# Optimization experiments

Hardware: AMD Instinct MI355X
Metric: run time of the kernel (lower is better)

The kernel has to match this reference:

```python
import jax, jax.numpy as jnp
import numpy as np

HIDDEN = 384
NDIM = 3
N_POINTS = 100000
N_SUPER = 2048
MAX_DEG = 32
RADIUS = 0.045
INPUT_DIM = 3


def _sincos_embed(coords):
    # ContinuousSincosEmbed: dim=384, ndim=3 -> 128 channels per spatial dim (64 sin + 64 cos)
    eff = HIDDEN // NDIM  # 128
    omega = jnp.arange(0, eff, 2, dtype=jnp.float32) / eff
    freq = 1.0 / (10000.0 ** omega)  # [eff//2]
    out = coords[..., None] * freq  # [..., ndim, eff//2]
    emb = jnp.concatenate([jnp.sin(out), jnp.cos(out)], axis=-1)  # [..., ndim, eff]
    return emb.reshape(coords.shape[:-1] + (HIDDEN,))


def _radius_neighbors(pos, sn_idx):
    # numpy preprocessing equivalent of torch_geometric.nn.pool.radius with
    # max_num_neighbors=MAX_DEG; fixed-size padded [S, K] output + validity mask.
    nbr = np.zeros((N_SUPER, MAX_DEG), np.int32)
    mask = np.zeros((N_SUPER, MAX_DEG), bool)
    pos2 = (pos ** 2).sum(-1)
    r2 = RADIUS * RADIUS
    chunk = 128
    for i0 in range(0, N_SUPER, chunk):
        sp = pos[sn_idx[i0:i0 + chunk]]
        d2 = (sp ** 2).sum(-1)[:, None] + pos2[None, :] - 2.0 * (sp @ pos.T)
        within = d2 <= r2
        for j in range(sp.shape[0]):
            idx = np.nonzero(within[j])[0][:MAX_DEG]
            nbr[i0 + j, :len(idx)] = idx
            mask[i0 + j, :len(idx)] = True
    return nbr, mask


def setup_inputs() -> dict:
    rng = np.random.default_rng(0)
    pos = rng.random((N_POINTS, NDIM)).astype(np.float32)
    sn_idx = np.sort(rng.choice(N_POINTS, N_SUPER, replace=False)).astype(np.int32)
    nbr, mask = _radius_neighbors(pos, sn_idx)
    key = jax.random.key(0)
    ks = jax.random.split(key, 6)
    s = 0.02  # truncnormal002 init scale
    return {
        "input_pos": jnp.asarray(pos),
        "input_feat": jax.random.normal(ks[0], (N_POINTS, INPUT_DIM), jnp.float32),
        "supernode_idx": jnp.asarray(sn_idx),
        "neighbor_idx": jnp.asarray(nbr),
        "neighbor_mask": jnp.asarray(mask),
        "W_in": jax.random.normal(ks[1], (INPUT_DIM, HIDDEN), jnp.float32) * s,
        "b_in": jnp.zeros((HIDDEN,), jnp.float32),
        "W1": jax.random.normal(ks[2], (2 * HIDDEN, HIDDEN), jnp.float32) * s,
        "b1": jnp.zeros((HIDDEN,), jnp.float32),
        "W2": jax.random.normal(ks[3], (HIDDEN, HIDDEN), jnp.float32) * s,
        "b2": jnp.zeros((HIDDEN,), jnp.float32),
        "W_proj": jax.random.normal(ks[4], (2 * HIDDEN, HIDDEN), jnp.float32) * s,
        "b_proj": jnp.zeros((HIDDEN,), jnp.float32),
    }


def reference(input_pos, input_feat, supernode_idx, neighbor_idx, neighbor_mask,
              W_in, b_in, W1, b1, W2, b2, W_proj, b_proj):
    # point embeddings: continuous sincos pos embed + input feature projection
    x = _sincos_embed(input_pos) + input_feat @ W_in + b_in          # [N, D]
    sn = x[supernode_idx]                                            # [S, D] supernode pos embed
    src = x[neighbor_idx]                                            # [S, K, D] gathered neighbors
    dst = jnp.broadcast_to(sn[:, None, :], src.shape)                # [S, K, D]
    h = jnp.concatenate([src, dst], axis=-1)                         # [S, K, 2D]
    # message MLP (Linear -> GELU(exact) -> Linear), as nn.GELU default
    h = jax.nn.gelu(h @ W1 + b1, approximate=False) @ W2 + b2        # [S, K, D]
    # masked mean == segment_csr(..., reduce='mean') over variable-degree edges
    m = neighbor_mask[..., None].astype(h.dtype)
    agg = (h * m).sum(axis=1) / jnp.maximum(m.sum(axis=1), 1.0)      # [S, D]
    # readd_supernode_pos: concat supernode pos embed, project 2D -> D
    out = jnp.concatenate([agg, sn], axis=-1) @ W_proj + b_proj      # [S, D]
    return out[None]                                                 # [1, S, D] (batch_size=1)
```

## Files before the change

kernel.cpp:

```cpp
#include <hip/hip_runtime.h>
#include <hip/hip_bf16.h>
#include <cstdint>

#define HIDDEN 384
#define NSUPER 2048
#define MAXDEG 32
#define FRAGS (12*24*64)
#define WBLK  (FRAGS*8)

typedef __attribute__((ext_vector_type(8))) short bf16x8;
typedef __attribute__((ext_vector_type(4))) float f32x4;

__device__ inline unsigned short f2bf(float f) {
    __hip_bfloat16 h = __float2bfloat16(f);
    return *reinterpret_cast<unsigned short*>(&h);
}
__device__ inline float b2f(unsigned short s) {
    return __uint_as_float(((unsigned int)s) << 16);
}
__device__ inline bf16x8 pack8(const float* v) {
    union { bf16x8 v8; unsigned short u[8]; } u;
    #pragma unroll
    for (int i = 0; i < 8; ++i) u.u[i] = f2bf(v[i]);
    return u.v8;
}
__device__ inline float fast_erf(float x) {
    float ax = fabsf(x);
    float t  = 1.0f / fmaf(0.3275911f, ax, 1.0f);
    float p  = t*(0.254829592f + t*(-0.284496736f + t*(1.421413741f +
               t*(-1.453152027f + t*1.061405429f))));
    float e  = __expf(-ax*ax);
    return copysignf(1.0f - p*e, x);
}
__device__ inline float gelu(float y) {
    return 0.5f * y * (1.0f + fast_erf(y * 0.70710678118654752f));
}

__global__ __launch_bounds__(256)
void prep(const float* __restrict__ W1, const float* __restrict__ W2,
          const float* __restrict__ Wp, const unsigned int* __restrict__ mask,
          const float* __restrict__ pos, const float* __restrict__ feat,
          const int* __restrict__ sn_idx,
          const float* __restrict__ W_in, const float* __restrict__ b_in,
          unsigned short* __restrict__ w1sf, unsigned short* __restrict__ w1df,
          unsigned short* __restrict__ w2f,  unsigned short* __restrict__ wpf,
          unsigned short* __restrict__ snxb, int* __restrict__ flag) {
    const int b = blockIdx.x;
    const int t = threadIdx.x;
    if (b == 360) {
        __shared__ int s;
        if (t == 0) s = 0;
        __syncthreads();
        int bad = 0;
        for (int i = t; i < 16384; i += 256)
            if (mask[i] > 1u) bad = 1;
        if (bad) s = 1;
        __syncthreads();
        if (t == 0) *flag = s;
        return;
    }
    if (b > 360) {
        __shared__ float W4[HIDDEN][4];
        __shared__ float P6[64][7];
        const int eb = b - 361;
        if (t < 64) {
            const int pi = sn_idx[eb*64 + t];
            P6[t][0]=pos[pi*3];  P6[t][1]=pos[pi*3+1];  P6[t][2]=pos[pi*3+2];
            P6[t][3]=feat[pi*3]; P6[t][4]=feat[pi*3+1]; P6[t][5]=feat[pi*3+2];
        }
        for (int d = t; d < HIDDEN; d += 256) {
            W4[d][0]=W_in[d]; W4[d][1]=W_in[HIDDEN+d];
            W4[d][2]=W_in[2*HIDDEN+d]; W4[d][3]=b_in[d];
        }
        __syncthreads();
        const int er = t >> 2, seg = t & 3;
        float frA[8], frB[8];
        #pragma unroll
        for (int i = 0; i < 8; ++i) {
            frA[i] = exp2f(-(float)(seg*8 + i)      * 0.2076205059304601f);
            frB[i] = exp2f(-(float)(32 + seg*8 + i) * 0.2076205059304601f);
        }
        const float f0 = P6[er][3], f1 = P6[er][4], f2 = P6[er][5];
        #pragma unroll
        for (int cc = 0; cc < 3; ++cc) {
            const float pc = P6[er][cc];
            float sL[8], sH[8], cL[8], cH[8];
            #pragma unroll
            for (int i = 0; i < 8; ++i) {
                const float aL = pc*frA[i], aH = pc*frB[i];
                sL[i]=__sinf(aL); sH[i]=__sinf(aH); cL[i]=__cosf(aL); cH[i]=__cosf(aH);
            }
            #pragma unroll
            for (int q = 0; q < 4; ++q) {
                const float* bb = (q==0)?sL:(q==1)?sH:(q==2)?cL:cH;
                const int blk = cc*4 + q;
                float v[8];
                #pragma unroll
                for (int i = 0; i < 8; ++i) {
                    const int dim = blk*32 + seg*8 + i;
                    const float4 wv = *(const float4*)W4[dim];
                    v[i] = fmaf(f0, wv.x, fmaf(f1, wv.y, fmaf(f2, wv.z, bb[i] + wv.w)));
                }
                *(bf16x8*)&snxb[(size_t)(eb*64 + er)*HIDDEN + blk*32 + seg*8] = pack8(v);
            }
        }
        return;
    }
    const int grp = b / 72, sub = b % 72;
    const float* W; unsigned short* out;
    switch (grp) {
        case 0: W = W1;              out = w1sf; break;
        case 1: W = W1 + 384*HIDDEN; out = w1df; break;
        case 2: W = W2;              out = w2f;  break;
        case 3: W = Wp;              out = wpf;  break;
        default:W = Wp + 384*HIDDEN; out = wpf + WBLK; break;
    }
    const int idx = sub * 256 + t;
    const int l   = idx & 63;
    const int frag= idx >> 6;
    const int nt  = frag % 24;
    const int kt  = frag / 24;
    const int col = nt * 16 + (l & 15);
    const int k0  = kt * 32 + (l >> 4) * 8;
    unsigned int pk[4];
    #pragma unroll
    for (int j = 0; j < 4; ++j) {
        unsigned int lo = f2bf(W[(k0 + 2*j)     * HIDDEN + col]);
        unsigned int hi = f2bf(W[(k0 + 2*j + 1) * HIDDEN + col]);
        pk[j] = lo | (hi << 16);
    }
    *reinterpret_cast<uint4*>(&out[(size_t)idx * 8]) =
        *reinterpret_cast<const uint4*>(pk);
}

__global__ __launch_bounds__(256)
void k_dstv(const unsigned short* __restrict__ snxb,
            const unsigned short* __restrict__ w1df,
            const float* __restrict__ b1, float* __restrict__ dstv) {
    const int rg = blockIdx.x >> 2, cq = blockIdx.x & 3;
    const int t = threadIdx.x, w = t>>6, l = t&63, lg = l>>4, l15 = l&15;
    const int wgm = w>>1, wgn = w&1;
    const int r0 = rg*64 + wgm*32;
    const int ntb = cq*6 + wgn*3;
    f32x4 acc[2][3];
    #pragma unroll
    for (int mt=0; mt<2; ++mt)
        #pragma unroll
        for (int nt=0; nt<3; ++nt) acc[mt][nt] = (f32x4){0.f,0.f,0.f,0.f};
    #pragma unroll 2
    for (int kt = 0; kt < 12; ++kt) {
        bf16x8 a[2], bfr[3];
        const unsigned short* bpp = &w1df[((size_t)(kt*24 + ntb)*64 + l)*8];
        #pragma unroll
        for (int nt=0; nt<3; ++nt) bfr[nt] = *(const bf16x8*)(bpp + (size_t)nt*512);
        #pragma unroll
        for (int mt=0; mt<2; ++mt)
            a[mt] = *(const bf16x8*)&snxb[(size_t)(r0 + mt*16 + l15)*HIDDEN + kt*32 + lg*8];
        #pragma unroll
        for (int mt=0; mt<2; ++mt)
            #pragma unroll
            for (int nt=0; nt<3; ++nt)
                acc[mt][nt] = __builtin_amdgcn_mfma_f32_16x16x32_bf16(a[mt], bfr[nt], acc[mt][nt], 0,0,0);
    }
    #pragma unroll
    for (int mt=0; mt<2; ++mt)
        #pragma unroll
        for (int nt=0; nt<3; ++nt) {
            const int col = cq*96 + wgn*48 + nt*16 + l15;
            #pragma unroll
            for (int r=0; r<4; ++r) {
                const int row = r0 + mt*16 + lg*4 + r;
                dstv[(size_t)row*HIDDEN + col] = acc[mt][nt][r] + b1[col];
            }
        }
}

__global__ __launch_bounds__(256, 2)
void k_mlp(const float* __restrict__ pos, const float* __restrict__ feat,
           const int* __restrict__ nbr_idx, const void* __restrict__ mask_raw,
           const int* __restrict__ mask_fmt,
           const float* __restrict__ W_in, const float* __restrict__ b_in,
           const float* __restrict__ dstv,
           const unsigned short* __restrict__ W1f,
           const unsigned short* __restrict__ W2f,
           const float* __restrict__ b2, unsigned short* __restrict__ aggb)
{
    __shared__ unsigned short G[4*12*64*8];
    __shared__ ushort4 WINTB[HIDDEN];
    __shared__ float PF[64][7];
    __shared__ float CNT[2];

    const int t  = threadIdx.x;
    const int bm = blockIdx.x;
    const int l = t & 63, ng = t >> 6, lg = l >> 4, l15 = l & 15;

    float dvreg[2][6];
    #pragma unroll
    for (int sl = 0; sl < 2; ++sl)
        #pragma unroll
        for (int nt = 0; nt < 6; ++nt)
            dvreg[sl][nt] = dstv[(size_t)(bm*2 + sl)*HIDDEN + ng*96 + nt*16 + l15];

    bf16x8 bA[6], bB[6];
    #define LOADB(dst, Wf, kt)                                                  \
        { const unsigned short* bp_ = &Wf[((size_t)((kt)*24 + ng*6)*64 + l)*8]; \
          _Pragma("unroll")                                                     \
          for (int nt_ = 0; nt_ < 6; ++nt_)                                     \
              dst[nt_] = *(const bf16x8*)(bp_ + (size_t)nt_*512); }
    #define AREAD(a_, kt)                                                       \
        { _Pragma("unroll")                                                     \
          for (int mt_ = 0; mt_ < 4; ++mt_)                                     \
              a_[mt_] = *(const bf16x8*)&G[(size_t)(((mt_*12 + (kt))*64) + l)*8]; }
    #define MFMA6(bfr, a_)                                                      \
        { __builtin_amdgcn_s_setprio(1);                                        \
          _Pragma("unroll")                                                     \
          for (int mt_ = 0; mt_ < 4; ++mt_)                                     \
              _Pragma("unroll")                                                 \
              for (int nt_ = 0; nt_ < 6; ++nt_)                                 \
                  acc[mt_][nt_] = __builtin_amdgcn_mfma_f32_16x16x32_bf16(      \
                      a_[mt_], bfr[nt_], acc[mt_][nt_], 0, 0, 0);               \
          __builtin_amdgcn_s_setprio(0); }

    LOADB(bA, W1f, 0); LOADB(bB, W1f, 1);

    if (t < 64) {
        const int e  = bm*64 + t;
        const int pi = nbr_idx[e];
        PF[t][0]=pos[pi*3];  PF[t][1]=pos[pi*3+1];  PF[t][2]=pos[pi*3+2];
        PF[t][3]=feat[pi*3]; PF[t][4]=feat[pi*3+1]; PF[t][5]=feat[pi*3+2];
        const int fmt = *mask_fmt;
        const int mv  = fmt ? (int)((const unsigned char*)mask_raw)[e]
                            : ((const int*)mask_raw)[e];
        PF[t][6] = mv ? 1.0f : 0.0f;
    }
    for (int d = t; d < HIDDEN; d += 256) {
        ushort4 wv;
        wv.x = f2bf(W_in[d]); wv.y = f2bf(W_in[HIDDEN+d]);
        wv.z = f2bf(W_in[2*HIDDEN+d]); wv.w = f2bf(b_in[d]);
        WINTB[d] = wv;
    }
    __syncthreads();
    if (t < 2) {
        float c = 0.f;
        for (int s = 0; s < 32; ++s) c += PF[t*32+s][6];
        CNT[t] = c;
    }

    {
        const int er = t >> 2, seg = t & 3;
        float frA[8], frB[8];
        #pragma unroll
        for (int i = 0; i < 8; ++i) {
            frA[i] = exp2f(-(float)(seg*8 + i)      * 0.2076205059304601f);
            frB[i] = exp2f(-(float)(32 + seg*8 + i) * 0.2076205059304601f);
        }
        const float f0 = PF[er][3], f1 = PF[er][4], f2 = PF[er][5];
        const int slotbase = (er>>4)*12*64 + seg*16 + (er&15);
        #pragma unroll
        for (int cc = 0; cc < 3; ++cc) {
            const float pc = PF[er][cc];
            float sL[8], sH[8], cL[8], cH[8];
            #pragma unroll
            for (int i = 0; i < 8; ++i) {
                const float aL = pc*frA[i], aH = pc*frB[i];
                sL[i]=__sinf(aL); sH[i]=__sinf(aH); cL[i]=__cosf(aL); cH[i]=__cosf(aH);
            }
            #pragma unroll
            for (int q = 0; q < 4; ++q) {
                const float* bb = (q==0)?sL:(q==1)?sH:(q==2)?cL:cH;
                const int blk = cc*4 + q;
                float v[8];
                #pragma unroll
                for (int i = 0; i < 8; ++i) {
                    const int dim = blk*32 + seg*8 + i;
                    const ushort4 wv = WINTB[dim];
                    v[i] = fmaf(f0, b2f(wv.x), fmaf(f1, b2f(wv.y),
                           fmaf(f2, b2f(wv.z), bb[i] + b2f(wv.w))));
                }
                *(bf16x8*)&G[(size_t)(slotbase + blk*64)*8] = pack8(v);
            }
        }
    }
    __syncthreads();

    f32x4 acc[4][6];

    #pragma unroll
    for (int mt=0; mt<4; ++mt)
        #pragma unroll
        for (int nt=0; nt<6; ++nt) acc[mt][nt] = (f32x4){0.f,0.f,0.f,0.f};
    #pragma unroll
    for (int kt = 0; kt < 12; kt += 2) {
        bf16x8 a[4];
        AREAD(a, kt);
        MFMA6(bA, a);
        if (kt + 2 < 12) LOADB(bA, W1f, kt + 2);
        AREAD(a, kt + 1);
        MFMA6(bB, a);
        if (kt + 3 < 12) LOADB(bB, W1f, kt + 3);
    }
    __syncthreads();

    #pragma unroll
    for (int mt=0; mt<4; ++mt) {
        const int sl = mt >> 1;
        #pragma unroll
        for (int nt=0; nt<6; ++nt) {
            const int col = ng*96 + nt*16 + l15;
            const float dv = dvreg[sl][nt];
            const int base = ((mt*12 + (col>>5))*64 + ((col>>3)&3)*16 + lg*4)*8 + (col&7);
            #pragma unroll
            for (int r=0; r<4; ++r)
                G[base + r*8] = f2bf(gelu(acc[mt][nt][r] + dv));
        }
    }
    __syncthreads();

    #pragma unroll
    for (int mt=0; mt<4; ++mt)
        #pragma unroll
        for (int nt=0; nt<6; ++nt) acc[mt][nt] = (f32x4){0.f,0.f,0.f,0.f};
    LOADB(bA, W2f, 0); LOADB(bB, W2f, 1);
    #pragma unroll
    for (int kt = 0; kt < 12; kt += 2) {
        bf16x8 a[4];
        AREAD(a, kt);
        MFMA6(bA, a);
        if (kt + 2 < 12) LOADB(bA, W2f, kt + 2);
        AREAD(a, kt + 1);
        MFMA6(bB, a);
        if (kt + 3 < 12) LOADB(bB, W2f, kt + 3);
    }

    #pragma unroll
    for (int nt=0; nt<6; ++nt) {
        const int col = ng*96 + nt*16 + l15;
        float s0 = 0.f, s1 = 0.f;
        #pragma unroll
        for (int mt=0; mt<4; ++mt) {
            float p = 0.f;
            #pragma unroll
            for (int r=0; r<4; ++r)
                p += PF[mt*16 + lg*4 + r][6] * acc[mt][nt][r];
            if (mt < 2) s0 += p; else s1 += p;
        }
        s0 += __shfl_xor(s0,16); s0 += __shfl_xor(s0,32);
        s1 += __shfl_xor(s1,16); s1 += __shfl_xor(s1,32);
        if (lg == 0) {
            const float bb = b2[col];
            const int sn0 = bm*2;
            const float c0 = CNT[0], c1 = CNT[1];
            aggb[(size_t)sn0*HIDDEN + col]     = f2bf(s0 / fmaxf(c0,1.f) + bb*(c0>0.f?1.f:0.f));
            aggb[(size_t)(sn0+1)*HIDDEN + col] = f2bf(s1 / fmaxf(c1,1.f) + bb*(c1>0.f?1.f:0.f));
        }
    }
    #undef LOADB
    #undef AREAD
    #undef MFMA6
}

__global__ __launch_bounds__(256)
void k_proj(const unsigned short* __restrict__ aggb,
            const unsigned short* __restrict__ snxb,
            const unsigned short* __restrict__ wpf,
            const float* __restrict__ bp, float* __restrict__ out) {
    const int rg = blockIdx.x >> 2, cq = blockIdx.x & 3;
    const int t = threadIdx.x, w = t>>6, l = t&63, lg = l>>4, l15 = l&15;
    const int wgm = w>>1, wgn = w&1;
    const int r0 = rg*64 + wgm*32;
    const int ntb = cq*6 + wgn*3;
    f32x4 acc[2][3];
    #pragma unroll
    for (int mt=0; mt<2; ++mt)
        #pragma unroll
        for (int nt=0; nt<3; ++nt) acc[mt][nt] = (f32x4){0.f,0.f,0.f,0.f};
    #pragma unroll 2
    for (int kt = 0; kt < 24; ++kt) {
        const unsigned short* Ab = (kt < 12) ? aggb : snxb;
        const unsigned short* Wb = (kt < 12) ? wpf  : wpf + WBLK;
        const int ktt = (kt < 12) ? kt : kt - 12;
        bf16x8 a[2], bfr[3];
        const unsigned short* bpp = &Wb[((size_t)(ktt*24 + ntb)*64 + l)*8];
        #pragma unroll
        for (int nt=0; nt<3; ++nt) bfr[nt] = *(const bf16x8*)(bpp + (size_t)nt*512);
        #pragma unroll
        for (int mt=0; mt<2; ++mt)
            a[mt] = *(const bf16x8*)&Ab[(size_t)(r0 + mt*16 + l15)*HIDDEN + ktt*32 + lg*8];
        #pragma unroll
        for (int mt=0; mt<2; ++mt)
            #pragma unroll
            for (int nt=0; nt<3; ++nt)
                acc[mt][nt] = __builtin_amdgcn_mfma_f32_16x16x32_bf16(a[mt], bfr[nt], acc[mt][nt], 0,0,0);
    }
    #pragma unroll
    for (int mt=0; mt<2; ++mt)
        #pragma unroll
        for (int nt=0; nt<3; ++nt) {
            const int col = cq*96 + wgn*48 + nt*16 + l15;
            #pragma unroll
            for (int r=0; r<4; ++r) {
                const int row = r0 + mt*16 + lg*4 + r;
                out[(size_t)row*HIDDEN + col] = acc[mt][nt][r] + bp[col];
            }
        }
}

extern "C" void kernel_launch(void* const* d_in, const int* in_sizes, int n_in,
                              void* d_out, int out_size, void* d_ws, size_t ws_size,
                              hipStream_t stream) {
    const float* pos   = (const float*)d_in[0];
    const float* feat  = (const float*)d_in[1];
    const int*   sn    = (const int*)d_in[2];
    const int*   nbr   = (const int*)d_in[3];
    const void*  mask  = d_in[4];
    const float* W_in  = (const float*)d_in[5];
    const float* b_in  = (const float*)d_in[6];
    const float* W1    = (const float*)d_in[7];
    const float* b1    = (const float*)d_in[8];
    const float* W2    = (const float*)d_in[9];
    const float* b2    = (const float*)d_in[10];
    const float* Wp    = (const float*)d_in[11];
    const float* bpv   = (const float*)d_in[12];
    float* out = (float*)d_out;

    char* base = (char*)d_ws;
    int* flag = (int*)base;
    unsigned short* w1sf = (unsigned short*)(base + 256);
    unsigned short* w1df = w1sf + WBLK;
    unsigned short* w2f  = w1df + WBLK;
    unsigned short* wpf  = w2f  + WBLK;
    unsigned short* snxb = wpf  + 2*(size_t)WBLK;
    unsigned short* aggb = snxb + (size_t)NSUPER*HIDDEN;
    float* dstv = (float*)(aggb + (size_t)NSUPER*HIDDEN);

    hipLaunchKernelGGL(prep, dim3(393), dim3(256), 0, stream,
                       W1, W2, Wp, (const unsigned int*)mask,
                       pos, feat, sn, W_in, b_in,
                       w1sf, w1df, w2f, wpf, snxb, flag);
    hipLaunchKernelGGL(k_dstv, dim3(128), dim3(256), 0, stream,
                       snxb, w1df, b1, dstv);
    hipLaunchKernelGGL(k_mlp, dim3(1024), dim3(256), 0, stream,
                       pos, feat, nbr, mask, flag, W_in, b_in, dstv, w1sf, w2f, b2, aggb);
    hipLaunchKernelGGL(k_proj, dim3(128), dim3(256), 0, stream,
                       aggb, snxb, wpf, bpv, out);
}
```

Before: 89.55 us.

## Interleave sincos embedding generation with first-layer MFMA K-loop

The sincos plus input-projection embedding is no longer computed for all 12 K-slices before the first GEMM. It is now generated one K-slice at a time inside the K loop, so the VALU transcendental work overlaps with the MFMA work on the previous slice. The intent is to hide embedding cost behind matrix-core time. In exchange it adds a __syncthreads per K-step (12 barriers instead of 1) and reduces W1 prefetch depth from two slices to one, which may expose load latency.

```diff
diff --git a/kernel.cpp b/kernel.cpp
--- a/kernel.cpp
+++ b/kernel.cpp
@@ -221,7 +221,7 @@
                       a_[mt_], bfr[nt_], acc[mt_][nt_], 0, 0, 0);               \
           __builtin_amdgcn_s_setprio(0); }
 
-    LOADB(bA, W1f, 0); LOADB(bB, W1f, 1);
+    LOADB(bA, W1f, 0);
 
     if (t < 64) {
         const int e  = bm*64 + t;
@@ -246,60 +246,53 @@
         CNT[t] = c;
     }
 
-    {
-        const int er = t >> 2, seg = t & 3;
-        float frA[8], frB[8];
-        #pragma unroll
-        for (int i = 0; i < 8; ++i) {
-            frA[i] = exp2f(-(float)(seg*8 + i)      * 0.2076205059304601f);
-            frB[i] = exp2f(-(float)(32 + seg*8 + i) * 0.2076205059304601f);
-        }
-        const float f0 = PF[er][3], f1 = PF[er][4], f2 = PF[er][5];
-        const int slotbase = (er>>4)*12*64 + seg*16 + (er&15);
-        #pragma unroll
-        for (int cc = 0; cc < 3; ++cc) {
-            const float pc = PF[er][cc];
-            float sL[8], sH[8], cL[8], cH[8];
-            #pragma unroll
-            for (int i = 0; i < 8; ++i) {
-                const float aL = pc*frA[i], aH = pc*frB[i];
-                sL[i]=__sinf(aL); sH[i]=__sinf(aH); cL[i]=__cosf(aL); cH[i]=__cosf(aH);
-            }
-            #pragma unroll
-            for (int q = 0; q < 4; ++q) {
-                const float* bb = (q==0)?sL:(q==1)?sH:(q==2)?cL:cH;
-                const int blk = cc*4 + q;
-                float v[8];
-                #pragma unroll
-                for (int i = 0; i < 8; ++i) {
-                    const int dim = blk*32 + seg*8 + i;
-                    const ushort4 wv = WINTB[dim];
-                    v[i] = fmaf(f0, b2f(wv.x), fmaf(f1, b2f(wv.y),
-                           fmaf(f2, b2f(wv.z), bb[i] + b2f(wv.w))));
-                }
-                *(bf16x8*)&G[(size_t)(slotbase + blk*64)*8] = pack8(v);
-            }
-        }
-    }
+    const int er = t >> 2, seg = t & 3;
+    float frA[8], frB[8];
+    #pragma unroll
+    for (int i = 0; i < 8; ++i) {
+        frA[i] = exp2f(-(float)(seg*8 + i)      * 0.2076205059304601f);
+        frB[i] = exp2f(-(float)(32 + seg*8 + i) * 0.2076205059304601f);
+    }
+    const float f0 = PF[er][3], f1 = PF[er][4], f2 = PF[er][5];
+    const float pc0 = PF[er][0], pc1 = PF[er][1], pc2 = PF[er][2];
+    const int slotbase = (er>>4)*12*64 + seg*16 + (er&15);
+
+    #define EMB(kt_)                                                            \
+        { const float pc = ((kt_)>>2)==0 ? pc0 : (((kt_)>>2)==1 ? pc1 : pc2);   \
+          float v[8];                                                           \
+          _Pragma("unroll")                                                     \
+          for (int i = 0; i < 8; ++i) {                                         \
+              const float fr = ((kt_)&1) ? frB[i] : frA[i];                     \
+              const float aa = pc * fr;                                         \
+              const float base = (((kt_)>>1)&1) ? __cosf(aa) : __sinf(aa);      \
+              const ushort4 wv = WINTB[(kt_)*32 + seg*8 + i];                   \
+              v[i] = fmaf(f0, b2f(wv.x), fmaf(f1, b2f(wv.y),                    \
+                     fmaf(f2, b2f(wv.z), base + b2f(wv.w))));                   \
+          }                                                                     \
+          *(bf16x8*)&G[(size_t)(slotbase + (kt_)*64)*8] = pack8(v); }
+
+    EMB(0);
     __syncthreads();
 
     f32x4 acc[4][6];
-
     #pragma unroll
     for (int mt=0; mt<4; ++mt)
         #pragma unroll
         for (int nt=0; nt<6; ++nt) acc[mt][nt] = (f32x4){0.f,0.f,0.f,0.f};
+
     #pragma unroll
     for (int kt = 0; kt < 12; kt += 2) {
         bf16x8 a[4];
         AREAD(a, kt);
+        LOADB(bB, W1f, kt + 1);
+        EMB(kt + 1);
         MFMA6(bA, a);
-        if (kt + 2 < 12) LOADB(bA, W1f, kt + 2);
+        __syncthreads();
         AREAD(a, kt + 1);
+        if (kt + 2 < 12) { LOADB(bA, W1f, kt + 2); EMB(kt + 2); }
         MFMA6(bB, a);
-        if (kt + 3 < 12) LOADB(bB, W1f, kt + 3);
-    }
-    __syncthreads();
+        __syncthreads();
+    }
 
     #pragma unroll
     for (int mt=0; mt<4; ++mt) {
@@ -357,6 +350,7 @@
     #undef LOADB
     #undef AREAD
     #undef MFMA6
+    #undef EMB
 }
 
 __global__ __launch_bounds__(256)
```

Result: no change. 90.24 us (+0.8%).
